# Optimization experiments

Measured on AMD Instinct MI355X. Metric: run time of the kernel, lower is better.

## Reference

```python
import jax, jax.numpy as jnp
import numpy as np

SR = 44100
LOWEST = 82.0
L_ORDER = 5
NUM_COEFF = L_ORDER + 1          # 6
NUM_ACTIVE = NUM_COEFF + 1       # 7 (linear interp)
K = int(SR // LOWEST) + NUM_ACTIVE  # coeff_vector_size = 544
N_FRAMES = 100
EXC_FRAMES = 100
EXC_ORDER = 5
BURST_LEN = 2048
N_SAMPLES = 44100


def upsample_linear(frames, T):
    """Linear interpolation of (F,) or (F, C) control frames to T samples (align_corners)."""
    F_ = frames.shape[0]
    pos = jnp.linspace(0.0, F_ - 1.0, T)
    i0 = jnp.clip(jnp.floor(pos).astype(jnp.int32), 0, F_ - 2)
    w = pos - i0.astype(pos.dtype)
    lo = frames[i0]
    hi = frames[i0 + 1]
    if frames.ndim == 2:
        w = w[:, None]
    return lo + (hi - lo) * w


def sample_wise_lpc(x, A):
    """Time-varying all-pole filter: y[t] = x[t] - sum_k A[t,k] * y[t-k-1].
    x: (T,), A: (T, N) -> y: (T,)"""
    N = A.shape[1]

    def step(buf, inp):
        xt, at = inp
        y = xt - jnp.dot(at, buf)  # buf[0]=y[t-1], ..., buf[N-1]=y[t-N]
        buf = jnp.concatenate([y[None], buf[:-1]])
        return buf, y

    _, y = jax.lax.scan(step, jnp.zeros((N,), x.dtype), (x, A))
    return y


def _forward(delay_len_frames, excitation, raw_coeff_frames, raw_gain, exc_coefficients, n_samples):
    T = n_samples
    # --- upsample control signals to audio rate ---
    delay = upsample_linear(delay_len_frames, T)                     # (T,)
    gain = jax.nn.sigmoid(raw_gain) * 0.1 + 0.9
    sb = jax.nn.sigmoid(raw_coeff_frames)                            # (F, 6)
    coeff_frames = sb / sb.sum(axis=-1, keepdims=True) * gain        # normalized, stable
    b = upsample_linear(coeff_frames, T)                             # (T, 6)

    # --- build sparse banded A (linear fractional-delay interpolation) ---
    z_l = jnp.floor(delay).astype(jnp.int32)                         # integer delay
    alfa = delay - z_l.astype(delay.dtype)                           # fractional part
    v0 = -(1.0 - alfa) * b[:, 0]                                     # (T,)
    vmid = -(alfa[:, None] * b[:, :-1] + (1.0 - alfa)[:, None] * b[:, 1:])  # (T, 5)
    vlast = -alfa * b[:, -1]                                         # (T,)
    vals = jnp.concatenate([v0[:, None], vmid, vlast[:, None]], axis=1)     # (T, 7)
    idxs = z_l[:, None] + jnp.arange(NUM_ACTIVE)[None, :]            # (T, 7)
    A = jnp.zeros((T, K), delay.dtype).at[jnp.arange(T)[:, None], idxs].set(vals)

    # --- excitation shaping filter (requires_grad branch) ---
    burst = excitation                                               # (BURST_LEN,)
    a_exc = upsample_linear(exc_coefficients, burst.shape[0])        # (BURST_LEN, 5)
    filtered_burst = sample_wise_lpc(burst, a_exc)

    # --- Karplus-Strong loop: time-varying all-pole with banded A ---
    x = jnp.zeros((T,), burst.dtype).at[: burst.shape[0]].set(filtered_burst)
    y = sample_wise_lpc(x, A)
    return y.astype(jnp.float32)


def setup_inputs() -> dict:
    key = jax.random.key(0)
    k0, k1, k2, k3 = jax.random.split(key, 4)
    # delay in [100, 520] samples so floor(delay)+NUM_ACTIVE-1 < K = 544
    delay_len_frames = 100.0 + 420.0 * jax.random.uniform(k0, (N_FRAMES,), dtype=jnp.float32)
    excitation = jax.random.normal(k1, (BURST_LEN,), dtype=jnp.float32)
    raw_coeff_frames = jax.random.uniform(k2, (N_FRAMES, NUM_COEFF), dtype=jnp.float32,
                                          minval=-2.0, maxval=0.0)
    raw_gain = jnp.asarray(0.0, dtype=jnp.float32)
    exc_coefficients = 0.01 * jax.random.normal(k3, (EXC_FRAMES, EXC_ORDER), dtype=jnp.float32)
    return {
        "delay_len_frames": delay_len_frames,
        "excitation": excitation,
        "raw_coeff_frames": raw_coeff_frames,
        "raw_gain": raw_gain,
        "exc_coefficients": exc_coefficients,
        "n_samples": N_SAMPLES,
    }


def reference(delay_len_frames, excitation, raw_coeff_frames, raw_gain, exc_coefficients, n_samples):
    return _forward(delay_len_frames, excitation, raw_coeff_frames, raw_gain,
                    exc_coefficients, n_samples)
```

## Files before the change

kernel.cpp:

```cpp
#include <hip/hip_runtime.h>
#include <math.h>


#define T_SAMPLES 44100
#define NFRAMES   100
#define NCOEF     6
#define NACT      7
#define BURST     2048
#define EXC_ORD   5

#define C2        100
#define HISTSZ    1096

#define WS_COEF_FLOATS (T_SAMPLES * 8)
#define WS_EXC_OFF     WS_COEF_FLOATS
#define WS_EXC_FLOATS  (EXC_ORD * BURST)
#define WS_TOTAL_BYTES ((size_t)(WS_COEF_FLOATS + WS_EXC_FLOATS) * 4)

__global__ __launch_bounds__(256) void diffks_precompute(
    const float* __restrict__ delay_frames,
    const float* __restrict__ raw_coeff,
    const float* __restrict__ raw_gain,
    const float* __restrict__ exc_coeff,
    float* __restrict__ ws)
{
    int g = blockIdx.x * 256 + threadIdx.x;
    const float gain = 0.1f / (1.0f + expf(-raw_gain[0])) + 0.9f;

    if (g < T_SAMPLES) {
        const float stepT = 99.0f / (float)(T_SAMPLES - 1);
        float pos = (float)g * stepT;
        int i0 = (int)pos; if (i0 > NFRAMES - 2) i0 = NFRAMES - 2;
        float w = pos - (float)i0;

        float d0 = delay_frames[i0], d1 = delay_frames[i0 + 1];
        float delay = d0 + (d1 - d0) * w;
        int z = (int)delay;
        float alfa = delay - (float)z;

        float b[NCOEF];
        {
            float c0v[NCOEF], c1v[NCOEF];
            float s0 = 0.f, s1 = 0.f;
            #pragma unroll
            for (int j = 0; j < NCOEF; ++j) {
                c0v[j] = 1.0f / (1.0f + expf(-raw_coeff[i0 * NCOEF + j]));
                c1v[j] = 1.0f / (1.0f + expf(-raw_coeff[(i0 + 1) * NCOEF + j]));
                s0 += c0v[j]; s1 += c1v[j];
            }
            float g0 = gain / s0, g1 = gain / s1;
            #pragma unroll
            for (int j = 0; j < NCOEF; ++j) {
                float x0 = c0v[j] * g0, x1 = c1v[j] * g1;
                b[j] = x0 + (x1 - x0) * w;
            }
        }
        float oma = 1.0f - alfa;
        float v0 = -oma * b[0];
        float v1 = -(alfa * b[0] + oma * b[1]);
        float v2 = -(alfa * b[1] + oma * b[2]);
        float v3 = -(alfa * b[2] + oma * b[3]);
        float v4 = -(alfa * b[3] + oma * b[4]);
        float v5 = -(alfa * b[4] + oma * b[5]);
        float v6 = -alfa * b[5];
        int base = g - z - 1;

        float4* o = (float4*)(ws + (size_t)g * 8);
        o[0] = make_float4(v0, v1, v2, v3);
        o[1] = make_float4(v4, v5, v6, __int_as_float(base));
    } else if (g < T_SAMPLES + BURST) {
        int te = g - T_SAMPLES;
        const float stepE = 99.0f / (float)(BURST - 1);
        float pos = (float)te * stepE;
        int i0 = (int)pos; if (i0 > NFRAMES - 2) i0 = NFRAMES - 2;
        float w = pos - (float)i0;
        float* o = ws + WS_EXC_OFF + te * EXC_ORD;
        #pragma unroll
        for (int k = 0; k < EXC_ORD; ++k) {
            float a0 = exc_coeff[i0 * EXC_ORD + k];
            float a1 = exc_coeff[(i0 + 1) * EXC_ORD + k];
            o[k] = a0 + (a1 - a0) * w;
        }
    }
}

__global__ __launch_bounds__(64, 1) void diffks_serial(
    const float* __restrict__ excitation,
    const float* __restrict__ ws,
    float* __restrict__ out)
{
    __shared__ float s_x[64][33];
    __shared__ float s_a[64][161];
    __shared__ float s_hist[HISTSZ];
    __shared__ float s_tail[64][32];
    __shared__ float s_bound[64][6];

    const int lane = threadIdx.x;

    for (int t = lane; t < BURST; t += 64)
        s_x[t >> 5][t & 31] = excitation[t];
    {
        for (int i = 0; i < 32; ++i) {
            int t = lane + i * 64;
            const float* g = ws + WS_EXC_OFF + t * EXC_ORD;
            float* dst = &s_a[t >> 5][(t & 31) * 5];
            dst[0] = g[0]; dst[1] = g[1]; dst[2] = g[2];
            dst[3] = g[3]; dst[4] = g[4];
        }
    }
    for (int i = lane; i < HISTSZ; i += 64) s_hist[i] = 0.0f;
    __syncthreads();

    {
        float st[6][5];
        #pragma unroll
        for (int r = 0; r < 6; ++r)
            #pragma unroll
            for (int k = 0; k < 5; ++k) st[r][k] = 0.0f;
        #pragma unroll
        for (int r = 1; r <= 5; ++r) st[r][r - 1] = 1.0f;

        const float* ar = &s_a[lane][0];
        const float* xr = &s_x[lane][0];
        #pragma unroll 8
        for (int i = 0; i < 32; ++i) {
            float a0 = ar[i * 5 + 0], a1 = ar[i * 5 + 1], a2 = ar[i * 5 + 2];
            float a3 = ar[i * 5 + 3], a4 = ar[i * 5 + 4];
            float xv = xr[i];
            #pragma unroll
            for (int r = 0; r < 6; ++r) {
                float acc = (r == 0) ? xv : 0.0f;
                acc = fmaf(-a0, st[r][0], acc);
                acc = fmaf(-a1, st[r][1], acc);
                acc = fmaf(-a2, st[r][2], acc);
                acc = fmaf(-a3, st[r][3], acc);
                acc = fmaf(-a4, st[r][4], acc);
                st[r][4] = st[r][3]; st[r][3] = st[r][2];
                st[r][2] = st[r][1]; st[r][1] = st[r][0];
                st[r][0] = acc;
            }
        }
        #pragma unroll
        for (int r = 0; r < 6; ++r)
            #pragma unroll
            for (int k = 0; k < 5; ++k)
                s_tail[lane][r * 5 + k] = st[r][k];
    }
    __syncthreads();

    if (lane == 0) {
        float Y[5] = {0.f, 0.f, 0.f, 0.f, 0.f};
        for (int l = 0; l < 64; ++l) {
            #pragma unroll
            for (int c = 0; c < 5; ++c) s_bound[l][c] = Y[c];
            float tl[30];
            #pragma unroll
            for (int j = 0; j < 30; ++j) tl[j] = s_tail[l][j];
            float ny[5];
            #pragma unroll
            for (int k = 0; k < 5; ++k) {
                float acc = tl[k];
                #pragma unroll
                for (int c = 1; c <= 5; ++c)
                    acc = fmaf(tl[c * 5 + k], Y[c - 1], acc);
                ny[k] = acc;
            }
            #pragma unroll
            for (int k = 0; k < 5; ++k) Y[k] = ny[k];
        }
    }
    __syncthreads();

    {
        float b0 = s_bound[lane][0], b1 = s_bound[lane][1], b2 = s_bound[lane][2];
        float b3 = s_bound[lane][3], b4 = s_bound[lane][4];
        const float* ar = &s_a[lane][0];
        float* xr = &s_x[lane][0];
        #pragma unroll 8
        for (int i = 0; i < 32; ++i) {
            float a0 = ar[i * 5 + 0], a1 = ar[i * 5 + 1], a2 = ar[i * 5 + 2];
            float a3 = ar[i * 5 + 3], a4 = ar[i * 5 + 4];
            float acc = xr[i];
            acc = fmaf(-a0, b0, acc);
            acc = fmaf(-a1, b1, acc);
            acc = fmaf(-a2, b2, acc);
            acc = fmaf(-a3, b3, acc);
            acc = fmaf(-a4, b4, acc);
            b4 = b3; b3 = b2; b2 = b1; b1 = b0; b0 = acc;
            xr[i] = acc;
        }
    }
    __syncthreads();

    const float4* cw = (const float4*)ws;
    const bool lane_act = (lane < 50);
    const unsigned dumpA = 1032u + (unsigned)lane;

    float4 CFq[8][4];
    #pragma unroll
    for (int j = 0; j < 8; ++j) {
        int tA = j * C2 + lane;
        int tB = tA + 50;
        CFq[j][0] = cw[tA * 2 + 0];
        CFq[j][1] = cw[tA * 2 + 1];
        CFq[j][2] = cw[tB * 2 + 0];
        CFq[j][3] = cw[tB * 2 + 1];
    }

    float hu[2][2][7];
    #pragma unroll
    for (int k = 0; k < 7; ++k) {
        hu[0][0][k] = 0.f; hu[0][1][k] = 0.f;
        hu[1][0][k] = 0.f; hu[1][1][k] = 0.f;
    }

    #define KS2_BODY(cc, j, WITHX, DO_NEXT)                                    \
    {                                                                          \
        const float4 a0 = CFq[j][0], a1 = CFq[j][1];                           \
        const float4 b0 = CFq[j][2], b1 = CFq[j][3];                           \
        const int tA = (cc) * C2 + lane;                                       \
        const int tB = tA + 50;                                                \
        float accA, accB;                                                      \
        if (WITHX) {                                                           \
            accA = (lane_act && tA < BURST) ? s_x[tA >> 5][tA & 31] : 0.0f;    \
            accB = (lane_act && tB < BURST) ? s_x[tB >> 5][tB & 31] : 0.0f;    \
        } else { accA = 0.0f; accB = 0.0f; }                                   \
        accA = fmaf(-a0.x, hu[(j) & 1][0][6], accA);                           \
        accB = fmaf(-b0.x, hu[(j) & 1][1][6], accB);                           \
        accA = fmaf(-a0.y, hu[(j) & 1][0][5], accA);                           \
        accB = fmaf(-b0.y, hu[(j) & 1][1][5], accB);                           \
        accA = fmaf(-a0.z, hu[(j) & 1][0][4], accA);                           \
        accB = fmaf(-b0.z, hu[(j) & 1][1][4], accB);                           \
        accA = fmaf(-a0.w, hu[(j) & 1][0][3], accA);                           \
        accB = fmaf(-b0.w, hu[(j) & 1][1][3], accB);                           \
        accA = fmaf(-a1.x, hu[(j) & 1][0][2], accA);                           \
        accB = fmaf(-b1.x, hu[(j) & 1][1][2], accB);                           \
        accA = fmaf(-a1.y, hu[(j) & 1][0][1], accA);                           \
        accB = fmaf(-b1.y, hu[(j) & 1][1][1], accB);                           \
        accA = fmaf(-a1.z, hu[(j) & 1][0][0], accA);                           \
        accB = fmaf(-b1.z, hu[(j) & 1][1][0], accB);                           \
        const unsigned pA = ((unsigned)tA) & 1023u;                            \
        const unsigned pB = ((unsigned)tB) & 1023u;                            \
        s_hist[lane_act ? pA : dumpA] = accA;                                  \
        s_hist[lane_act ? pB : dumpA] = accB;                                  \
        s_hist[(lane_act && pA < 7u) ? (pA + 1024u) : dumpA] = accA;           \
        s_hist[(lane_act && pB < 7u) ? (pB + 1024u) : dumpA] = accB;           \
        if (DO_NEXT) {                                                         \
            int nbA = __float_as_int(CFq[((j) + 1) & 7][1].w);                 \
            int nbB = __float_as_int(CFq[((j) + 1) & 7][3].w);                 \
            unsigned qA = ((unsigned)(nbA - 6)) & 1023u;                       \
            unsigned qB = ((unsigned)(nbB - 6)) & 1023u;                       \
            hu[((j) & 1) ^ 1][0][0] = s_hist[qA + 0];                          \
            hu[((j) & 1) ^ 1][0][1] = s_hist[qA + 1];                          \
            hu[((j) & 1) ^ 1][0][2] = s_hist[qA + 2];                          \
            hu[((j) & 1) ^ 1][0][3] = s_hist[qA + 3];                          \
            hu[((j) & 1) ^ 1][0][4] = s_hist[qA + 4];                          \
            hu[((j) & 1) ^ 1][0][5] = s_hist[qA + 5];                          \
            hu[((j) & 1) ^ 1][0][6] = s_hist[qA + 6];                          \
            hu[((j) & 1) ^ 1][1][0] = s_hist[qB + 0];                          \
            hu[((j) & 1) ^ 1][1][1] = s_hist[qB + 1];                          \
            hu[((j) & 1) ^ 1][1][2] = s_hist[qB + 2];                          \
            hu[((j) & 1) ^ 1][1][3] = s_hist[qB + 3];                          \
            hu[((j) & 1) ^ 1][1][4] = s_hist[qB + 4];                          \
            hu[((j) & 1) ^ 1][1][5] = s_hist[qB + 5];                          \
            hu[((j) & 1) ^ 1][1][6] = s_hist[qB + 6];                          \
            int tA8 = ((cc) + 8) * C2 + lane;                                  \
            if (tA8 > T_SAMPLES - 1) tA8 = T_SAMPLES - 1;                      \
            int tB8 = tA8 + 50;                                                \
            if (tB8 > T_SAMPLES - 1) tB8 = T_SAMPLES - 1;                      \
            CFq[j][0] = cw[tA8 * 2 + 0];                                       \
            CFq[j][1] = cw[tA8 * 2 + 1];                                       \
            CFq[j][2] = cw[tB8 * 2 + 0];                                       \
            CFq[j][3] = cw[tB8 * 2 + 1];                                       \
        }                                                                      \
    }

    #define DUMP800(g)                                                         \
    {                                                                          \
        const int t0 = (g) * 800;                                              \
        _Pragma("unroll")                                                      \
        for (int i = 0; i < 12; ++i) {                                         \
            int t = t0 + i * 64 + lane;                                        \
            out[t] = s_hist[((unsigned)t) & 1023u];                            \
        }                                                                      \
        {                                                                      \
            int t = t0 + 768 + lane;                                           \
            if (lane < 32) out[t] = s_hist[((unsigned)t) & 1023u];             \
        }                                                                      \
    }

    #pragma unroll 1
    for (int g = 0; g < 3; ++g) {
        const int cb = g * 8;
        KS2_BODY(cb + 0, 0, true, true)
        KS2_BODY(cb + 1, 1, true, true)
        KS2_BODY(cb + 2, 2, true, true)
        KS2_BODY(cb + 3, 3, true, true)
        KS2_BODY(cb + 4, 4, true, true)
        KS2_BODY(cb + 5, 5, true, true)
        KS2_BODY(cb + 6, 6, true, true)
        KS2_BODY(cb + 7, 7, true, true)
        DUMP800(g)
    }
    #pragma unroll 1
    for (int g = 3; g < 55; ++g) {
        const int cb = g * 8;
        KS2_BODY(cb + 0, 0, false, true)
        KS2_BODY(cb + 1, 1, false, true)
        KS2_BODY(cb + 2, 2, false, true)
        KS2_BODY(cb + 3, 3, false, true)
        KS2_BODY(cb + 4, 4, false, true)
        KS2_BODY(cb + 5, 5, false, true)
        KS2_BODY(cb + 6, 6, false, true)
        KS2_BODY(cb + 7, 7, false, true)
        DUMP800(g)
    }
    KS2_BODY(440, 0, false, false)
    {
        int t = 44000 + lane;
        out[t] = s_hist[((unsigned)t) & 1023u];
        int t2 = t + 64;
        if (lane < 36) out[t2] = s_hist[((unsigned)t2) & 1023u];
    }
    #undef KS2_BODY
    #undef DUMP800
}

#define CHUNK_FB  101
#define NCH_FB    ((T_SAMPLES + CHUNK_FB - 1) / CHUNK_FB)
#define HIST_FB   1024

__global__ __launch_bounds__(128) void diffks_fallback(
    const float* __restrict__ delay_frames,
    const float* __restrict__ excitation,
    const float* __restrict__ raw_coeff,
    const float* __restrict__ raw_gain,
    const float* __restrict__ exc_coeff,
    float* __restrict__ out)
{
    __shared__ float s_a[EXC_ORD][BURST];
    __shared__ float s_x[BURST];
    __shared__ float s_hist[HIST_FB];
    __shared__ __align__(16) float s_coef[NFRAMES][8];
    __shared__ float s_delay[NFRAMES];

    const int tid = threadIdx.x;
    const float gain = 0.1f / (1.0f + expf(-raw_gain[0])) + 0.9f;

    for (int i = tid; i < NFRAMES; i += 128) s_delay[i] = delay_frames[i];
    for (int f = tid; f < NFRAMES; f += 128) {
        float sb[NCOEF]; float s = 0.0f;
        #pragma unroll
        for (int j = 0; j < NCOEF; ++j) {
            sb[j] = 1.0f / (1.0f + expf(-raw_coeff[f * NCOEF + j]));
            s += sb[j];
        }
        float inv = gain / s;
        #pragma unroll
        for (int j = 0; j < NCOEF; ++j) s_coef[f][j] = sb[j] * inv;
        s_coef[f][6] = 0.0f; s_coef[f][7] = 0.0f;
    }
    const float stepE = 99.0f / 2047.0f;
    for (int t = tid; t < BURST; t += 128) {
        float pos = (float)t * stepE;
        int i0 = (int)pos; if (i0 > NFRAMES - 2) i0 = NFRAMES - 2;
        float w = pos - (float)i0;
        const float* c0 = exc_coeff + i0 * EXC_ORD;
        #pragma unroll
        for (int k = 0; k < EXC_ORD; ++k) {
            float a0 = c0[k], a1 = c0[k + EXC_ORD];
            s_a[k][t] = a0 + (a1 - a0) * w;
        }
        s_x[t] = excitation[t];
    }
    for (int i = tid; i < HIST_FB; i += 128) s_hist[i] = 0.0f;
    __syncthreads();

    if (tid == 0) {
        float y1 = 0.f, y2 = 0.f, y3 = 0.f, y4 = 0.f, y5 = 0.f;
        #pragma unroll 4
        for (int t = 0; t < BURST; ++t) {
            float p = s_x[t];
            p = fmaf(-s_a[1][t], y2, p);
            p = fmaf(-s_a[2][t], y3, p);
            p = fmaf(-s_a[3][t], y4, p);
            p = fmaf(-s_a[4][t], y5, p);
            float y = fmaf(-s_a[0][t], y1, p);
            s_x[t] = y;
            y5 = y4; y4 = y3; y3 = y2; y2 = y1; y1 = y;
        }
    }
    __syncthreads();

    const float stepT = 99.0f / (float)(T_SAMPLES - 1);
    for (int c = 0; c < NCH_FB; ++c) {
        int t = c * CHUNK_FB + tid;
        if (tid < CHUNK_FB && t < T_SAMPLES) {
            float pos = (float)t * stepT;
            int i0 = (int)pos; if (i0 > NFRAMES - 2) i0 = NFRAMES - 2;
            float w = pos - (float)i0;
            float d0 = s_delay[i0], d1 = s_delay[i0 + 1];
            float delay = d0 + (d1 - d0) * w;
            int z = (int)delay;
            float alfa = delay - (float)z;
            const float4* f0 = reinterpret_cast<const float4*>(s_coef[i0]);
            const float4* f1 = reinterpret_cast<const float4*>(s_coef[i0 + 1]);
            float4 c0a = f0[0], c0b = f0[1];
            float4 c1a = f1[0], c1b = f1[1];
            float b[NCOEF];
            b[0] = c0a.x + (c1a.x - c0a.x) * w;
            b[1] = c0a.y + (c1a.y - c0a.y) * w;
            b[2] = c0a.z + (c1a.z - c0a.z) * w;
            b[3] = c0a.w + (c1a.w - c0a.w) * w;
            b[4] = c0b.x + (c1b.x - c0b.x) * w;
            b[5] = c0b.y + (c1b.y - c0b.y) * w;
            float oma = 1.0f - alfa;
            float v[NACT];
            v[0] = -oma * b[0];
            #pragma unroll
            for (int j = 1; j <= 5; ++j) v[j] = -(alfa * b[j - 1] + oma * b[j]);
            v[6] = -alfa * b[5];
            float x = (t < BURST) ? s_x[t] : 0.0f;
            int base = t - z - 1;
            float sum = 0.0f;
            #pragma unroll
            for (int j = 0; j < NACT; ++j) {
                int idx = base - j;
                float yv = s_hist[idx & (HIST_FB - 1)];
                if (idx < 0) yv = 0.0f;
                sum = fmaf(v[j], yv, sum);
            }
            float y = x - sum;
            s_hist[t & (HIST_FB - 1)] = y;
            out[t] = y;
        }
        __syncthreads();
    }
}

extern "C" void kernel_launch(void* const* d_in, const int* in_sizes, int n_in,
                              void* d_out, int out_size, void* d_ws, size_t ws_size,
                              hipStream_t stream) {
    const float* delay_frames = (const float*)d_in[0];
    const float* excitation   = (const float*)d_in[1];
    const float* raw_coeff    = (const float*)d_in[2];
    const float* raw_gain     = (const float*)d_in[3];
    const float* exc_coeff    = (const float*)d_in[4];
    float* out = (float*)d_out;

    if (ws_size >= WS_TOTAL_BYTES) {
        float* ws = (float*)d_ws;
        int gridA = (T_SAMPLES + BURST + 255) / 256;
        diffks_precompute<<<gridA, 256, 0, stream>>>(delay_frames, raw_coeff,
                                                     raw_gain, exc_coeff, ws);
        diffks_serial<<<1, 64, 0, stream>>>(excitation, ws, out);
    } else {
        diffks_fallback<<<1, 128, 0, stream>>>(delay_frames, excitation,
                                               raw_coeff, raw_gain, exc_coeff, out);
    }
}
```

Measured before the change: 174.4 us.

## Stage per-group coefficients into LDS via async global_load_lds double buffering

The serial recurrence kernel used to keep an 8-deep register queue of float4 coefficient loads issued straight from global memory. It now copies each 800-sample group of coefficients into a double-buffered LDS array with the async global-to-LDS load builtin, issued once per group. It waits on vmcnt before the buffer is consumed and fetches coefficients from LDS two steps ahead. The aim is to take global-load latency off the single-wave critical path and free registers, at the cost of extra LDS traffic and explicit waitcnt synchronisation.

After: 183.2 us. 5.0% more time.

```diff
diff --git a/kernel.cpp b/kernel.cpp
--- a/kernel.cpp
+++ b/kernel.cpp
@@ -11,6 +11,7 @@
 
 #define C2        100
 #define HISTSZ    1096
+#define CFPAD     6528
 
 #define WS_COEF_FLOATS (T_SAMPLES * 8)
 #define WS_EXC_OFF     WS_COEF_FLOATS
@@ -84,11 +85,19 @@
     }
 }
 
+__device__ __forceinline__ void gload_lds16(const float* g, float* l) {
+    __builtin_amdgcn_global_load_lds(
+        (const __attribute__((address_space(1))) unsigned int*)(g),
+        (__attribute__((address_space(3))) unsigned int*)(l),
+        16, 0, 0);
+}
+
 __global__ __launch_bounds__(64, 1) void diffks_serial(
     const float* __restrict__ excitation,
     const float* __restrict__ ws,
     float* __restrict__ out)
 {
+    __shared__ float s_cf[2][CFPAD];
     __shared__ float s_x[64][33];
     __shared__ float s_a[64][161];
     __shared__ float s_hist[HISTSZ];
@@ -192,19 +201,32 @@
     }
     __syncthreads();
 
-    const float4* cw = (const float4*)ws;
     const bool lane_act = (lane < 50);
     const unsigned dumpA = 1032u + (unsigned)lane;
 
-    float4 CFq[8][4];
-    #pragma unroll
-    for (int j = 0; j < 8; ++j) {
-        int tA = j * C2 + lane;
-        int tB = tA + 50;
-        CFq[j][0] = cw[tA * 2 + 0];
-        CFq[j][1] = cw[tA * 2 + 1];
-        CFq[j][2] = cw[tB * 2 + 0];
-        CFq[j][3] = cw[tB * 2 + 1];
+    #define STAGE_GRP(gg)                                                      \
+    {                                                                          \
+        float* dstb = s_cf[(gg) & 1];                                          \
+        const float* srcb = ws + (size_t)(gg) * 6400 + lane * 4;               \
+        const int nis = ((gg) == 55) ? 4 : 25;                                 \
+        for (int i = 0; i < nis; ++i)                                          \
+            gload_lds16(srcb + i * 256, dstb + i * 256);                       \
+    }
+
+    STAGE_GRP(0)
+    asm volatile("s_waitcnt vmcnt(0)" ::: "memory");
+
+    float4 CF4[4][4];
+    {
+        const float4* cfp = (const float4*)s_cf[0];
+        #pragma unroll
+        for (int b = 0; b < 2; ++b) {
+            int lb = b * 100 + lane;
+            CF4[b][0] = cfp[lb * 2 + 0];
+            CF4[b][1] = cfp[lb * 2 + 1];
+            CF4[b][2] = cfp[(lb + 50) * 2 + 0];
+            CF4[b][3] = cfp[(lb + 50) * 2 + 1];
+        }
     }
 
     float hu[2][2][7];
@@ -214,11 +236,11 @@
         hu[1][0][k] = 0.f; hu[1][1][k] = 0.f;
     }
 
-    #define KS2_BODY(cc, j, WITHX, DO_NEXT)                                    \
+    #define KS3_BODY(j, WITHX, DO_NEXT)                                        \
     {                                                                          \
-        const float4 a0 = CFq[j][0], a1 = CFq[j][1];                           \
-        const float4 b0 = CFq[j][2], b1 = CFq[j][3];                           \
-        const int tA = (cc) * C2 + lane;                                       \
+        const float4 a0 = CF4[(j) & 3][0], a1 = CF4[(j) & 3][1];               \
+        const float4 b0 = CF4[(j) & 3][2], b1 = CF4[(j) & 3][3];               \
+        const int tA = cb100 + (j) * 100 + lane;                               \
         const int tB = tA + 50;                                                \
         float accA, accB;                                                      \
         if (WITHX) {                                                           \
@@ -246,32 +268,35 @@
         s_hist[(lane_act && pA < 7u) ? (pA + 1024u) : dumpA] = accA;           \
         s_hist[(lane_act && pB < 7u) ? (pB + 1024u) : dumpA] = accB;           \
         if (DO_NEXT) {                                                         \
-            int nbA = __float_as_int(CFq[((j) + 1) & 7][1].w);                 \
-            int nbB = __float_as_int(CFq[((j) + 1) & 7][3].w);                 \
+            int nbA = __float_as_int(CF4[((j) + 1) & 3][1].w);                 \
+            int nbB = __float_as_int(CF4[((j) + 1) & 3][3].w);                 \
             unsigned qA = ((unsigned)(nbA - 6)) & 1023u;                       \
             unsigned qB = ((unsigned)(nbB - 6)) & 1023u;                       \
-            hu[((j) & 1) ^ 1][0][0] = s_hist[qA + 0];                          \
-            hu[((j) & 1) ^ 1][0][1] = s_hist[qA + 1];                          \
-            hu[((j) & 1) ^ 1][0][2] = s_hist[qA + 2];                          \
-            hu[((j) & 1) ^ 1][0][3] = s_hist[qA + 3];                          \
-            hu[((j) & 1) ^ 1][0][4] = s_hist[qA + 4];                          \
-            hu[((j) & 1) ^ 1][0][5] = s_hist[qA + 5];                          \
-            hu[((j) & 1) ^ 1][0][6] = s_hist[qA + 6];                          \
-            hu[((j) & 1) ^ 1][1][0] = s_hist[qB + 0];                          \
-            hu[((j) & 1) ^ 1][1][1] = s_hist[qB + 1];                          \
-            hu[((j) & 1) ^ 1][1][2] = s_hist[qB + 2];                          \
-            hu[((j) & 1) ^ 1][1][3] = s_hist[qB + 3];                          \
-            hu[((j) & 1) ^ 1][1][4] = s_hist[qB + 4];                          \
-            hu[((j) & 1) ^ 1][1][5] = s_hist[qB + 5];                          \
-            hu[((j) & 1) ^ 1][1][6] = s_hist[qB + 6];                          \
-            int tA8 = ((cc) + 8) * C2 + lane;                                  \
-            if (tA8 > T_SAMPLES - 1) tA8 = T_SAMPLES - 1;                      \
-            int tB8 = tA8 + 50;                                                \
-            if (tB8 > T_SAMPLES - 1) tB8 = T_SAMPLES - 1;                      \
-            CFq[j][0] = cw[tA8 * 2 + 0];                                       \
-            CFq[j][1] = cw[tA8 * 2 + 1];                                       \
-            CFq[j][2] = cw[tB8 * 2 + 0];                                       \
-            CFq[j][3] = cw[tB8 * 2 + 1];                                       \
+            const float* hbA = &s_hist[qA];                                    \
+            const float* hbB = &s_hist[qB];                                    \
+            hu[((j) & 1) ^ 1][0][0] = hbA[0];                                  \
+            hu[((j) & 1) ^ 1][0][1] = hbA[1];                                  \
+            hu[((j) & 1) ^ 1][0][2] = hbA[2];                                  \
+            hu[((j) & 1) ^ 1][0][3] = hbA[3];                                  \
+            hu[((j) & 1) ^ 1][0][4] = hbA[4];                                  \
+            hu[((j) & 1) ^ 1][0][5] = hbA[5];                                  \
+            hu[((j) & 1) ^ 1][0][6] = hbA[6];                                  \
+            hu[((j) & 1) ^ 1][1][0] = hbB[0];                                  \
+            hu[((j) & 1) ^ 1][1][1] = hbB[1];                                  \
+            hu[((j) & 1) ^ 1][1][2] = hbB[2];                                  \
+            hu[((j) & 1) ^ 1][1][3] = hbB[3];                                  \
+            hu[((j) & 1) ^ 1][1][4] = hbB[4];                                  \
+            hu[((j) & 1) ^ 1][1][5] = hbB[5];                                  \
+            hu[((j) & 1) ^ 1][1][6] = hbB[6];                                  \
+            {                                                                  \
+                const float4* cfp =                                            \
+                    (const float4*)(((j) + 2 < 8) ? cfc : cfn);                \
+                const int lb = (((j) + 2) & 7) * 100 + lane;                   \
+                CF4[((j) + 2) & 3][0] = cfp[lb * 2 + 0];                       \
+                CF4[((j) + 2) & 3][1] = cfp[lb * 2 + 1];                       \
+                CF4[((j) + 2) & 3][2] = cfp[(lb + 50) * 2 + 0];                \
+                CF4[((j) + 2) & 3][3] = cfp[(lb + 50) * 2 + 1];                \
+            }                                                                  \
         }                                                                      \
     }
 
@@ -291,39 +316,54 @@
 
     #pragma unroll 1
     for (int g = 0; g < 3; ++g) {
-        const int cb = g * 8;
-        KS2_BODY(cb + 0, 0, true, true)
-        KS2_BODY(cb + 1, 1, true, true)
-        KS2_BODY(cb + 2, 2, true, true)
-        KS2_BODY(cb + 3, 3, true, true)
-        KS2_BODY(cb + 4, 4, true, true)
-        KS2_BODY(cb + 5, 5, true, true)
-        KS2_BODY(cb + 6, 6, true, true)
-        KS2_BODY(cb + 7, 7, true, true)
+        float* cfc = s_cf[g & 1];
+        float* cfn = s_cf[(g & 1) ^ 1];
+        const int cb100 = g * 800;
+        KS3_BODY(0, true, true)
+        STAGE_GRP(g + 1)
+        KS3_BODY(1, true, true)
+        KS3_BODY(2, true, true)
+        KS3_BODY(3, true, true)
+        KS3_BODY(4, true, true)
+        KS3_BODY(5, true, true)
+        asm volatile("s_waitcnt vmcnt(0)" ::: "memory");
+        KS3_BODY(6, true, true)
+        KS3_BODY(7, true, true)
         DUMP800(g)
     }
     #pragma unroll 1
     for (int g = 3; g < 55; ++g) {
-        const int cb = g * 8;
-        KS2_BODY(cb + 0, 0, false, true)
-        KS2_BODY(cb + 1, 1, false, true)
-        KS2_BODY(cb + 2, 2, false, true)
-        KS2_BODY(cb + 3, 3, false, true)
-        KS2_BODY(cb + 4, 4, false, true)
-        KS2_BODY(cb + 5, 5, false, true)
-        KS2_BODY(cb + 6, 6, false, true)
-        KS2_BODY(cb + 7, 7, false, true)
+        float* cfc = s_cf[g & 1];
+        float* cfn = s_cf[(g & 1) ^ 1];
+        const int cb100 = g * 800;
+        KS3_BODY(0, false, true)
+        STAGE_GRP(g + 1)
+        KS3_BODY(1, false, true)
+        KS3_BODY(2, false, true)
+        KS3_BODY(3, false, true)
+        KS3_BODY(4, false, true)
+        KS3_BODY(5, false, true)
+        asm volatile("s_waitcnt vmcnt(0)" ::: "memory");
+        KS3_BODY(6, false, true)
+        KS3_BODY(7, false, true)
         DUMP800(g)
     }
-    KS2_BODY(440, 0, false, false)
+    {
+        float* cfc = s_cf[1];
+        float* cfn = s_cf[0];
+        const int cb100 = 44000;
+        (void)cfc; (void)cfn;
+        KS3_BODY(0, false, false)
+    }
     {
         int t = 44000 + lane;
         out[t] = s_hist[((unsigned)t) & 1023u];
         int t2 = t + 64;
         if (lane < 36) out[t2] = s_hist[((unsigned)t2) & 1023u];
     }
-    #undef KS2_BODY
+    #undef KS3_BODY
     #undef DUMP800
+    #undef STAGE_GRP
 }
 
 #define CHUNK_FB  101
```
